# Performance work log

Hardware: AMD Instinct MI355X
Metric: run time of the kernel (lower is better)

Reference implementation:

```python
import jax, jax.numpy as jnp
import numpy as np

DIM = 512  # module's self.dim, used for the softmax scale (note: NOT head dim)

def setup_inputs() -> dict:
    key = jax.random.key(0)
    kq, kk, kv = jax.random.split(key, 3)
    shape = (4, 8, 2048, 64)  # [B, H, S, Dh]
    q = jax.random.normal(kq, shape, dtype=jnp.float32)
    k = jax.random.normal(kk, shape, dtype=jnp.float32)
    v = jax.random.normal(kv, shape, dtype=jnp.float32)
    return {"q": q, "k": k, "v": v, "n": 2048}

def reference(q, k, v, n):
    # scores = q @ k^T, then divide by sqrt(dim) AFTER matmul (as in source)
    scores = jnp.einsum('bhqd,bhkd->bhqk', q, k)
    scale = jnp.sqrt(jnp.asarray(DIM, dtype=scores.dtype))
    p_attn = jax.nn.softmax(scores / scale, axis=-1)
    return jnp.einsum('bhqk,bhkd->bhqd', p_attn, v)
```

## Files before the change

### kernel.cpp

```cpp
#include <hip/hip_runtime.h>


using half8   = __attribute__((ext_vector_type(8))) _Float16;
using half4   = __attribute__((ext_vector_type(4))) _Float16;
using half2v  = __attribute__((ext_vector_type(2))) _Float16;
using f32x4   = __attribute__((ext_vector_type(4))) float;
using f32x16  = __attribute__((ext_vector_type(16))) float;
using int4v   = __attribute__((ext_vector_type(4))) int;

static __device__ __forceinline__ half2v cvt_pk(float a, float b) {
    return __builtin_bit_cast(half2v, __builtin_amdgcn_cvt_pkrtz(a, b));
}
static __device__ __forceinline__ int cvt_pk_i(float a, float b) {
    return __builtin_bit_cast(int, __builtin_amdgcn_cvt_pkrtz(a, b));
}

#define SEQ   2048
#define DH    64
#define QB    128
#define KVB   64
#define NKVT  (SEQ / KVB)
#define NQB   (SEQ / QB)
#define NBH   32
#define TILE_IMG_BYTES 16384
#define QSCALE (1.4426950408889634f / 22.627416997969522f)

#if __has_builtin(__builtin_amdgcn_exp2f)
#define EXP2F __builtin_amdgcn_exp2f
#else
#define EXP2F exp2f
#endif

#define GLDS(gp, lp)                                                      \
    __builtin_amdgcn_global_load_lds(                                     \
        (const __attribute__((address_space(1))) void*)(gp),              \
        (__attribute__((address_space(3))) void*)(lp), 16, 0, 0)

#define WAIT_VM(N)                                             \
    do {                                                       \
        asm volatile("s_waitcnt vmcnt(" #N ")" ::: "memory");  \
        __builtin_amdgcn_sched_barrier(0);                     \
    } while (0)

#define WAIT_LGKM(N)                                           \
    do {                                                       \
        asm volatile("s_waitcnt lgkmcnt(" #N ")" ::: "memory");\
        __builtin_amdgcn_sched_barrier(0);                     \
    } while (0)

#define PLSWAP(a, b) \
    asm volatile("s_nop 1\n\tv_permlane32_swap_b32 %0, %1" : "+v"(a), "+v"(b))

#define MFMA32(A, B, C) __builtin_amdgcn_mfma_f32_32x32x16_f16((A), (B), (C), 0, 0, 0)

static __device__ __forceinline__ f32x16 z16() {
    f32x16 v;
#pragma unroll
    for (int i = 0; i < 16; ++i) v[i] = 0.f;
    return v;
}

#define SOFTPACK16(ST, PA, LSUM)                                          \
    do {                                                                  \
        float p[16];                                                      \
        _Pragma("unroll")                                                 \
        for (int r = 0; r < 16; ++r) p[r] = EXP2F((ST)[r]);               \
        float s0 = 0.f, s1 = 0.f;                                         \
        _Pragma("unroll")                                                 \
        for (int r = 0; r < 8; ++r) { s0 += p[r]; s1 += p[r + 8]; }       \
        (LSUM) += s0 + s1;                                                \
        int m0 = cvt_pk_i(p[0],  p[1]),  m1 = cvt_pk_i(p[2],  p[3]);      \
        int m2 = cvt_pk_i(p[4],  p[5]),  m3 = cvt_pk_i(p[6],  p[7]);      \
        int m4 = cvt_pk_i(p[8],  p[9]),  m5 = cvt_pk_i(p[10], p[11]);     \
        int m6 = cvt_pk_i(p[12], p[13]), m7 = cvt_pk_i(p[14], p[15]);     \
        PLSWAP(m0, m2); PLSWAP(m1, m3);                                   \
        PLSWAP(m4, m6); PLSWAP(m5, m7);                                   \
        int4v t0; t0[0] = m0; t0[1] = m1; t0[2] = m2; t0[3] = m3;         \
        int4v t1; t1[0] = m4; t1[1] = m5; t1[2] = m6; t1[3] = m7;         \
        (PA)[0] = __builtin_bit_cast(half8, t0);                          \
        (PA)[1] = __builtin_bit_cast(half8, t1);                          \
    } while (0)

#define STEP(STP0, STP1, STN0, STN1, VFP, VFN, T)                          \
    do {                                                                   \
        WAIT_LGKM(0);                     \
        WAIT_VM(0);                             \
        __builtin_amdgcn_s_barrier();     \
        if ((T) + 1 < NKVT) stage((T) + 1, ((T) & 1) ^ 1);                 \
        const char* kb_ = KVl[(T) & 1];                                    \
        half8 kf_[8];                                                      \
        _Pragma("unroll")                                                  \
        for (int j = 0; j < 8; ++j)                                        \
            kf_[j] = *(const half8*)(kb_ + j * 1024 + lane * 16);          \
        __builtin_amdgcn_sched_barrier(0);                                 \
        _Pragma("unroll")                                                  \
        for (int j = 0; j < 8; ++j)                                        \
            (VFN)[j] = *(const half8*)(kb_ + 8192 + j * 1024 + lane * 16); \
        __builtin_amdgcn_sched_barrier(0);  \
        half8 PA_[4];                                                      \
        SOFTPACK16(STP0, PA_,     lsum);       \
        SOFTPACK16(STP1, PA_ + 2, lsum);                                   \
        WAIT_LGKM(8);                       \
        __builtin_amdgcn_s_setprio(1);                                     \
        (STN0) = MFMA32(kf_[0], qfrag[0], ZV);                             \
        (STN1) = MFMA32(kf_[4], qfrag[0], ZV);                             \
        acc0   = MFMA32(PA_[0], (VFP)[0], acc0);                           \
        acc1   = MFMA32(PA_[0], (VFP)[4], acc1);                           \
        _Pragma("unroll")                                                  \
        for (int ks = 1; ks < 4; ++ks) {                                   \
            (STN0) = MFMA32(kf_[ks],     qfrag[ks], (STN0));               \
            (STN1) = MFMA32(kf_[4 + ks], qfrag[ks], (STN1));               \
            acc0   = MFMA32(PA_[ks], (VFP)[ks],     acc0);                 \
            acc1   = MFMA32(PA_[ks], (VFP)[4 + ks], acc1);                 \
        }                                                                  \
        __builtin_amdgcn_s_setprio(0);                                     \
    } while (0)

__global__ __launch_bounds__(256)
void prep_kv(const float* __restrict__ Kg, const float* __restrict__ Vg,
             char* __restrict__ ws)
{
    __shared__ __align__(16) _Float16 Kl[64][72];
    __shared__ __align__(16) _Float16 Vt[64][72];

    const int bid = blockIdx.x;
    const int bh  = bid >> 5;
    const int kvt = bid & 31;
    const int tid = threadIdx.x;

    const float* kg = Kg + ((size_t)bh * SEQ + (size_t)kvt * 64) * DH;
    const float* vg = Vg + ((size_t)bh * SEQ + (size_t)kvt * 64) * DH;
#pragma unroll
    for (int rr = 0; rr < 4; ++rr) {
        int row = rr * 16 + (tid >> 4);
        int c4  = (tid & 15) * 4;
        f32x4 kk = *(const f32x4*)(kg + (size_t)row * DH + c4);
        f32x4 vv = *(const f32x4*)(vg + (size_t)row * DH + c4);
#pragma unroll
        for (int j = 0; j < 4; ++j) {
            Kl[row][c4 + j] = (_Float16)kk[j];
            Vt[c4 + j][row] = (_Float16)vv[j];
        }
    }
    __syncthreads();

    char* out = ws + (size_t)bid * TILE_IMG_BYTES;
#pragma unroll
    for (int rep = 0; rep < 2; ++rep) {
        int f    = rep * 256 + tid;
        int ln   = f & 63;
        int ks   = (f >> 6) & 3;
        int g2   = f >> 8;
        int row  = g2 * 32 + (ln & 31);
        int colh = ks * 16 + (ln >> 5) * 8;
        *(half8*)(out + f * 16)        = *(const half8*)&Kl[row][colh];
        *(half8*)(out + 8192 + f * 16) = *(const half8*)&Vt[row][colh];
    }
}

__global__ __launch_bounds__(256, 2)
void fattn_fwd(const float* __restrict__ Qg, const char* __restrict__ Wimg,
               float* __restrict__ Og)
{
    __shared__ __align__(16) char KVl[2][TILE_IMG_BYTES];

    const int tid  = threadIdx.x;
    const int lane = tid & 63;
    const int wave = tid >> 6;
    const int l31  = lane & 31;
    const int hi   = lane >> 5;

    const int wg  = blockIdx.x;
    const int swz = (wg & 7) * 64 + (wg >> 3);
    const int qb  = swz & (NQB - 1);
    const int bh  = swz >> 4;
    const size_t base = (size_t)bh * (SEQ * DH);

    half8 qfrag[4];
    {
        const int qrow = qb * QB + wave * 32 + l31;
        const float* qp = Qg + base + (size_t)qrow * DH + hi * 8;
#pragma unroll
        for (int ks = 0; ks < 4; ++ks) {
            f32x4 a = *(const f32x4*)(qp + ks * 16);
            f32x4 b = *(const f32x4*)(qp + ks * 16 + 4);
            half8 f;
#pragma unroll
            for (int i = 0; i < 4; ++i) f[i]     = (_Float16)(a[i] * QSCALE);
#pragma unroll
            for (int i = 0; i < 4; ++i) f[i + 4] = (_Float16)(b[i] * QSCALE);
            qfrag[ks] = f;
        }
    }

    f32x16 acc0 = z16(), acc1 = z16();
    const f32x16 ZV = z16();
    float lsum = 0.f;

    const char* imgbase = Wimg + (size_t)(bh * NKVT) * TILE_IMG_BYTES;
    const int sfrag = wave * 4;

    auto stage = [&](int kvt, int b) {
        const char* g = imgbase + (size_t)kvt * TILE_IMG_BYTES
                        + sfrag * 1024 + lane * 16;
        char* l = &KVl[b][sfrag * 1024];
        GLDS(g,        l);
        GLDS(g + 1024, l + 1024);
        GLDS(g + 2048, l + 2048);
        GLDS(g + 3072, l + 3072);
    };

    f32x16 stE0, stE1, stO0, stO1;
    half8 vfE[8], vfO[8];

    stage(0, 0);
    WAIT_VM(0);
    __builtin_amdgcn_s_barrier();
    stage(1, 1);
    {
        const char* kb0 = KVl[0];
        half8 kf0[8];
#pragma unroll
        for (int j = 0; j < 8; ++j)
            kf0[j] = *(const half8*)(kb0 + j * 1024 + lane * 16);
        __builtin_amdgcn_sched_barrier(0);
#pragma unroll
        for (int j = 0; j < 8; ++j)
            vfE[j] = *(const half8*)(kb0 + 8192 + j * 1024 + lane * 16);
        WAIT_LGKM(8);
        __builtin_amdgcn_s_setprio(1);
        stE0 = MFMA32(kf0[0], qfrag[0], ZV);
        stE1 = MFMA32(kf0[4], qfrag[0], ZV);
#pragma unroll
        for (int ks = 1; ks < 4; ++ks) {
            stE0 = MFMA32(kf0[ks],     qfrag[ks], stE0);
            stE1 = MFMA32(kf0[4 + ks], qfrag[ks], stE1);
        }
        __builtin_amdgcn_s_setprio(0);
    }

#pragma unroll 1
    for (int t = 1; t + 1 < NKVT; t += 2) {
        STEP(stE0, stE1, stO0, stO1, vfE, vfO, t);
        STEP(stO0, stO1, stE0, stE1, vfO, vfE, t + 1);
    }
    STEP(stE0, stE1, stO0, stO1, vfE, vfO, NKVT - 1);

    WAIT_LGKM(0);
    {
        half8 PF[4];
        SOFTPACK16(stO0, PF,     lsum);
        SOFTPACK16(stO1, PF + 2, lsum);
        __builtin_amdgcn_s_setprio(1);
#pragma unroll
        for (int ks = 0; ks < 4; ++ks) {
            acc0 = MFMA32(PF[ks], vfO[ks],     acc0);
            acc1 = MFMA32(PF[ks], vfO[4 + ks], acc1);
        }
        __builtin_amdgcn_s_setprio(0);
    }

    lsum += __shfl_xor(lsum, 32);
    const float invl = 1.f / lsum;
    const int qstrip = qb * QB + wave * 32;
#pragma unroll
    for (int r = 0; r < 16; ++r) {
        int q16 = (r & 3) + 8 * (r >> 2) + 4 * hi;
        float sc = __shfl(invl, q16);
        float* op = Og + base + (size_t)(qstrip + q16) * DH;
        op[l31]      = acc0[r] * sc;
        op[32 + l31] = acc1[r] * sc;
    }
}

extern "C" void kernel_launch(void* const* d_in, const int* in_sizes, int n_in,
                              void* d_out, int out_size, void* d_ws, size_t ws_size,
                              hipStream_t stream) {
    const float* q = (const float*)d_in[0];
    const float* k = (const float*)d_in[1];
    const float* v = (const float*)d_in[2];
    float* o = (float*)d_out;
    char* ws = (char*)d_ws;
    prep_kv<<<dim3(NBH * NKVT, 1, 1), dim3(256, 1, 1), 0, stream>>>(k, v, ws);
    fattn_fwd<<<dim3(NQB * NBH, 1, 1), dim3(256, 1, 1), 0, stream>>>(q, ws, o);
}
```

Measured before the change: 57.43 us.

## Deepen KV pipeline to 4 LDS buffers and prefetch next K fragments to registers

Grows the shared K/V staging ring from two to four tiles so global-to-LDS loads run two tiles ahead. K fragments for the next tile are read into registers one step early, so the QK^T MFMAs no longer wait on LDS reads issued in the same step, and the per-step lgkm wait-all is dropped. The prologue is folded into the STEP macro with a FIRST flag. In exchange LDS use doubles to 64 KB per block and register pressure rises from the extra K fragment arrays, which may lower occupancy below the requested two blocks per CU.

```diff
diff --git a/kernel.cpp b/kernel.cpp
--- a/kernel.cpp
+++ b/kernel.cpp
@@ -81,37 +81,48 @@
         (PA)[1] = __builtin_bit_cast(half8, t1);                          \
     } while (0)
 
-#define STEP(STP0, STP1, STN0, STN1, VFP, VFN, T)                          \
+#define STEP(STP0, STP1, STN0, STN1, KF_C, KF_N, VF_C, VF_N, T, FIRST)     \
     do {                                                                   \
-        WAIT_LGKM(0);                     \
-        WAIT_VM(0);                             \
-        __builtin_amdgcn_s_barrier();     \
-        if ((T) + 1 < NKVT) stage((T) + 1, ((T) & 1) ^ 1);                 \
-        const char* kb_ = KVl[(T) & 1];                                    \
-        half8 kf_[8];                                                      \
-        _Pragma("unroll")                                                  \
-        for (int j = 0; j < 8; ++j)                                        \
-            kf_[j] = *(const half8*)(kb_ + j * 1024 + lane * 16);          \
-        __builtin_amdgcn_sched_barrier(0);                                 \
-        _Pragma("unroll")                                                  \
-        for (int j = 0; j < 8; ++j)                                        \
-            (VFN)[j] = *(const half8*)(kb_ + 8192 + j * 1024 + lane * 16); \
-        __builtin_amdgcn_sched_barrier(0);  \
+        WAIT_VM(0);                    \
+        __builtin_amdgcn_s_barrier();  \
+                                       \
+        if ((T) + 2 < NKVT) stage((T) + 2);                                \
+        {                                                                  \
+            const char* kbn_ = KVl[((T) + 1) & 3];                         \
+            const char* kbv_ = KVl[(T) & 3];                               \
+            if ((T) + 1 < NKVT) {                                          \
+                _Pragma("unroll")                                          \
+                for (int j = 0; j < 8; ++j)                                \
+                    (KF_N)[j] = *(const half8*)(kbn_ + j * 1024 + lane * 16); \
+            }                                                              \
+            __builtin_amdgcn_sched_barrier(0);                             \
+            _Pragma("unroll")                                              \
+            for (int j = 0; j < 8; ++j)                                    \
+                (VF_N)[j] = *(const half8*)(kbv_ + 8192 + j * 1024 + lane * 16); \
+            __builtin_amdgcn_sched_barrier(0);                             \
+        }                                                                  \
         half8 PA_[4];                                                      \
-        SOFTPACK16(STP0, PA_,     lsum);       \
-        SOFTPACK16(STP1, PA_ + 2, lsum);                                   \
-        WAIT_LGKM(8);                       \
+        if (!(FIRST)) {                                                    \
+            SOFTPACK16(STP0, PA_,     lsum);                               \
+            SOFTPACK16(STP1, PA_ + 2, lsum);                               \
+        }                                                                  \
+        WAIT_LGKM(8);                  \
+                                       \
         __builtin_amdgcn_s_setprio(1);                                     \
-        (STN0) = MFMA32(kf_[0], qfrag[0], ZV);                             \
-        (STN1) = MFMA32(kf_[4], qfrag[0], ZV);                             \
-        acc0   = MFMA32(PA_[0], (VFP)[0], acc0);                           \
-        acc1   = MFMA32(PA_[0], (VFP)[4], acc1);                           \
+        (STN0) = MFMA32((KF_C)[0], qfrag[0], ZV);                          \
+        (STN1) = MFMA32((KF_C)[4], qfrag[0], ZV);                          \
+        if (!(FIRST)) {                                                    \
+            acc0 = MFMA32(PA_[0], (VF_C)[0], acc0);                        \
+            acc1 = MFMA32(PA_[0], (VF_C)[4], acc1);                        \
+        }                                                                  \
         _Pragma("unroll")                                                  \
         for (int ks = 1; ks < 4; ++ks) {                                   \
-            (STN0) = MFMA32(kf_[ks],     qfrag[ks], (STN0));               \
-            (STN1) = MFMA32(kf_[4 + ks], qfrag[ks], (STN1));               \
-            acc0   = MFMA32(PA_[ks], (VFP)[ks],     acc0);                 \
-            acc1   = MFMA32(PA_[ks], (VFP)[4 + ks], acc1);                 \
+            (STN0) = MFMA32((KF_C)[ks],     qfrag[ks], (STN0));            \
+            (STN1) = MFMA32((KF_C)[4 + ks], qfrag[ks], (STN1));            \
+            if (!(FIRST)) {                                                \
+                acc0 = MFMA32(PA_[ks], (VF_C)[ks],     acc0);              \
+                acc1 = MFMA32(PA_[ks], (VF_C)[4 + ks], acc1);              \
+            }                                                              \
         }                                                                  \
         __builtin_amdgcn_s_setprio(0);                                     \
     } while (0)
@@ -162,7 +173,7 @@
 void fattn_fwd(const float* __restrict__ Qg, const char* __restrict__ Wimg,
                float* __restrict__ Og)
 {
-    __shared__ __align__(16) char KVl[2][TILE_IMG_BYTES];
+    __shared__ __align__(16) char KVl[4][TILE_IMG_BYTES];
 
     const int tid  = threadIdx.x;
     const int lane = tid & 63;
@@ -200,51 +211,36 @@
     const char* imgbase = Wimg + (size_t)(bh * NKVT) * TILE_IMG_BYTES;
     const int sfrag = wave * 4;
 
-    auto stage = [&](int kvt, int b) {
+    auto stage = [&](int kvt) {
         const char* g = imgbase + (size_t)kvt * TILE_IMG_BYTES
                         + sfrag * 1024 + lane * 16;
-        char* l = &KVl[b][sfrag * 1024];
+        char* l = &KVl[kvt & 3][sfrag * 1024];
         GLDS(g,        l);
         GLDS(g + 1024, l + 1024);
         GLDS(g + 2048, l + 2048);
         GLDS(g + 3072, l + 3072);
     };
 
+    half8  kfE[8], kfO[8], vfE[8], vfO[8];
     f32x16 stE0, stE1, stO0, stO1;
-    half8 vfE[8], vfO[8];
-
-    stage(0, 0);
+
+    stage(0);
+    stage(1);
     WAIT_VM(0);
     __builtin_amdgcn_s_barrier();
-    stage(1, 1);
-    {
-        const char* kb0 = KVl[0];
-        half8 kf0[8];
-#pragma unroll
-        for (int j = 0; j < 8; ++j)
-            kf0[j] = *(const half8*)(kb0 + j * 1024 + lane * 16);
-        __builtin_amdgcn_sched_barrier(0);
-#pragma unroll
-        for (int j = 0; j < 8; ++j)
-            vfE[j] = *(const half8*)(kb0 + 8192 + j * 1024 + lane * 16);
-        WAIT_LGKM(8);
-        __builtin_amdgcn_s_setprio(1);
-        stE0 = MFMA32(kf0[0], qfrag[0], ZV);
-        stE1 = MFMA32(kf0[4], qfrag[0], ZV);
-#pragma unroll
-        for (int ks = 1; ks < 4; ++ks) {
-            stE0 = MFMA32(kf0[ks],     qfrag[ks], stE0);
-            stE1 = MFMA32(kf0[4 + ks], qfrag[ks], stE1);
-        }
-        __builtin_amdgcn_s_setprio(0);
-    }
+#pragma unroll
+    for (int j = 0; j < 8; ++j)
+        kfE[j] = *(const half8*)(KVl[0] + j * 1024 + lane * 16);
+    WAIT_LGKM(0);
+
+    STEP(stO0, stO1, stE0, stE1, kfE, kfO, vfO, vfE, 0, true);
 
 #pragma unroll 1
-    for (int t = 1; t + 1 < NKVT; t += 2) {
-        STEP(stE0, stE1, stO0, stO1, vfE, vfO, t);
-        STEP(stO0, stO1, stE0, stE1, vfO, vfE, t + 1);
-    }
-    STEP(stE0, stE1, stO0, stO1, vfE, vfO, NKVT - 1);
+    for (int t = 1; t < 31; t += 2) {
+        STEP(stE0, stE1, stO0, stO1, kfO, kfE, vfE, vfO, t, false);
+        STEP(stO0, stO1, stE0, stE1, kfE, kfO, vfO, vfE, t + 1, false);
+    }
+    STEP(stE0, stE1, stO0, stO1, kfO, kfE, vfE, vfO, 31, false);
 
     WAIT_LGKM(0);
     {
```

Measured after the change: 63.62 us. +10.8%, slower.
